# Kernel optimization log

Measured on AMD Instinct MI355X. Metric: run time of the kernel, lower is better.

The kernel has to match this reference:

```python
import jax, jax.numpy as jnp
import numpy as np

# operators = ["min" (T-norm, no_edge offset = 1), "max" (T-conorm, no_edge offset = 0)]
# edge_types = ["identity", "complement", "no_edge"]
NO_EDGE_OFFSET_T_NORM = 1.0
NO_EDGE_OFFSET_T_CONORM = 0.0


def setup_inputs() -> dict:
    key = jax.random.key(0)
    k1, k2, k3 = jax.random.split(key, 3)
    N, IN, OUT, OPS, E = 1024, 512, 256, 2, 3
    eps = 1e-6
    return {
        "x": jax.random.uniform(k1, (N, IN), jnp.float32),
        "edge_logits": jnp.ones((OUT, OPS, IN, E), jnp.float32),
        "op_logits": jnp.ones((OUT, OPS), jnp.float32),
        "u_edge": jax.random.uniform(k2, (OUT, OPS, IN, E), jnp.float32, minval=eps, maxval=1.0 - eps),
        "u_op": jax.random.uniform(k3, (OUT, OPS), jnp.float32, minval=eps, maxval=1.0 - eps),
    }


def _gumbel_softmax_hard(logits, u, axis=-1):
    # Straight-through hard Gumbel-softmax (tau=1), reparameterized with uniform noise u.
    g = -jnp.log(-jnp.log(u))
    y_soft = jax.nn.softmax(logits + g, axis=axis)
    idx = jnp.argmax(y_soft, axis=axis)
    y_hard = jax.nn.one_hot(idx, logits.shape[axis], axis=axis, dtype=y_soft.dtype)
    return y_hard + y_soft - jax.lax.stop_gradient(y_soft)


def reference(x, edge_logits, op_logits, u_edge, u_op):
    # x: [N, I] fuzzy memberships in [0, 1]
    op_edge_sel = _gumbel_softmax_hard(edge_logits, u_edge)  # [O, P, I, E]
    op_sel = _gumbel_softmax_hard(op_logits, u_op)           # [O, P]
    op_idx = jnp.argmax(op_sel, axis=-1)                     # [O], 0 -> min (T-norm), 1 -> max (T-conorm)

    # edge_selection = op_edge_selection[range(O), op_idx]   -> [O, I, E]
    edge_sel = jnp.take_along_axis(op_edge_sel, op_idx[:, None, None, None], axis=1)[:, 0]

    is_tnorm = (op_idx == 0)
    no_edge_off = jnp.where(is_tnorm, NO_EDGE_OFFSET_T_NORM, NO_EDGE_OFFSET_T_CONORM).astype(x.dtype)  # [O]

    # edge type values: identity = x, complement = 1 - x, no_edge = 0 (+ operator offset)
    # edge_values[n, o, i] = max_e edge_sel[o, i, e] * etv[n, o, i, e]
    ev = edge_sel[None, :, :, 0] * x[:, None, :]                          # identity   [N, O, I]
    ev = jnp.maximum(ev, edge_sel[None, :, :, 1] * (1.0 - x)[:, None, :])  # complement
    ev = jnp.maximum(ev, edge_sel[None, :, :, 2] * no_edge_off[None, :, None])  # no_edge

    # operator.value over incoming edges: min for T-norm nodes, max for T-conorm nodes
    mn = jnp.min(ev, axis=-1)  # [N, O]
    mx = jnp.max(ev, axis=-1)  # [N, O]
    return jnp.where(is_tnorm[None, :], mn, mx)
```

## Files before the change

### kernel.cpp

```cpp
#include <hip/hip_runtime.h>
#include <math.h>

#define N_   1024
#define IN_  512
#define OUT_ 256
#define E_   3

__global__ __launch_bounds__(256) void setup_op_kernel(
        const float* __restrict__ op_logits,
        const float* __restrict__ u_op,
        int*   __restrict__ opidx,
        float* __restrict__ signv,
        float* __restrict__ neutral) {
    int o = threadIdx.x;
    float s0 = op_logits[o * 2 + 0] - logf(-logf(u_op[o * 2 + 0]));
    float s1 = op_logits[o * 2 + 1] - logf(-logf(u_op[o * 2 + 1]));
    int p = (s1 > s0) ? 1 : 0;
    opidx[o] = p;
    signv[o] = (p == 0) ? 1.0f : -1.0f;
    neutral[o] = (p == 0) ? 1.0f : 0.0f;
}

__global__ __launch_bounds__(256) void setup_coef_kernel(
        const float* __restrict__ edge_logits,
        const float* __restrict__ u_edge,
        const int*   __restrict__ opidx,
        const float* __restrict__ signv,
        const float* __restrict__ neutral,
        unsigned int* __restrict__ coefT) {
    int o = threadIdx.x;
    int i = blockIdx.x;
    int p = opidx[o];
    long base = (((long)(o * 2 + p)) * IN_ + i) * E_;

    float best = -1e30f;
    int be = 0;
#pragma unroll
    for (int e = 0; e < E_; ++e) {
        float u = u_edge[base + e];
        float sc = edge_logits[base + e] - logf(-logf(u));
        if (sc > best) { best = sc; be = e; }
    }
    float s = signv[o];
    float a, b;
    if (be == 0)      { a = s;    b = 0.0f; }
    else if (be == 1) { a = -s;   b = s;    }
    else              { a = 0.0f; b = s * neutral[o]; }

    unsigned int ua = (__float_as_uint(a) >> 16);
    unsigned int ub = (__float_as_uint(b) & 0xffff0000u);
    coefT[i * OUT_ + o] = ua | ub;
}

template <int NPB, int ISTEPS>
__global__ __launch_bounds__(256) void main_kernel(
        const float* __restrict__ x,
        const unsigned int* __restrict__ coefT,
        const float* __restrict__ signv,
        float* __restrict__ outp,
        int write_final) {
    constexpr int NSPLIT = IN_ / ISTEPS;
    int tid = threadIdx.x;
    int bid = blockIdx.x;
    int ks = bid % NSPLIT;
    int nt = bid / NSPLIT;
    int n0 = nt * NPB;
    int i0 = ks * ISTEPS;

    __shared__ float xT[ISTEPS * NPB];

    for (int k = tid; k < ISTEPS * NPB; k += 256) {
        int r = k / ISTEPS;
        int ii = k % ISTEPS;
        xT[ii * NPB + r] = x[(n0 + r) * IN_ + i0 + ii];
    }
    __syncthreads();

    float acc[NPB];
#pragma unroll
    for (int r = 0; r < NPB; ++r) acc[r] = 2.0f;

    const unsigned int* cp = coefT + (long)i0 * OUT_ + tid;

#pragma unroll 4
    for (int ii = 0; ii < ISTEPS; ++ii) {
        unsigned int c = cp[(long)ii * OUT_];
        float a = __uint_as_float(c << 16);
        float b = __uint_as_float(c & 0xffff0000u);
        const float4* xv = (const float4*)&xT[ii * NPB];
        float4 x0 = xv[0];
        float4 x1 = xv[1];
        acc[0] = fminf(acc[0], fmaf(a, x0.x, b));
        acc[1] = fminf(acc[1], fmaf(a, x0.y, b));
        acc[2] = fminf(acc[2], fmaf(a, x0.z, b));
        acc[3] = fminf(acc[3], fmaf(a, x0.w, b));
        acc[4] = fminf(acc[4], fmaf(a, x1.x, b));
        acc[5] = fminf(acc[5], fmaf(a, x1.y, b));
        acc[6] = fminf(acc[6], fmaf(a, x1.z, b));
        acc[7] = fminf(acc[7], fmaf(a, x1.w, b));
    }

    if (write_final) {
        float s = signv[tid];
#pragma unroll
        for (int r = 0; r < NPB; ++r)
            outp[(n0 + r) * OUT_ + tid] = s * acc[r];
    } else {
#pragma unroll
        for (int r = 0; r < NPB; ++r)
            outp[((long)ks * N_ + (n0 + r)) * OUT_ + tid] = acc[r];
    }
}

__global__ __launch_bounds__(256) void reduce_kernel(
        const float* __restrict__ partial,
        const float* __restrict__ signv,
        float* __restrict__ out,
        int nsplit) {
    int j = blockIdx.x * 256 + threadIdx.x;
    float m = partial[j];
    for (int k = 1; k < nsplit; ++k)
        m = fminf(m, partial[(long)k * (N_ * OUT_) + j]);
    out[j] = signv[j & (OUT_ - 1)] * m;
}

extern "C" void kernel_launch(void* const* d_in, const int* in_sizes, int n_in,
                              void* d_out, int out_size, void* d_ws, size_t ws_size,
                              hipStream_t stream) {
    const float* x           = (const float*)d_in[0];
    const float* edge_logits = (const float*)d_in[1];
    const float* op_logits   = (const float*)d_in[2];
    const float* u_edge      = (const float*)d_in[3];
    const float* u_op        = (const float*)d_in[4];
    float* out = (float*)d_out;

    char* ws = (char*)d_ws;
    int*   opidx   = (int*)(ws);
    float* signv   = (float*)(ws + 1024);
    float* neutral = (float*)(ws + 2048);
    unsigned int* coefT = (unsigned int*)(ws + 4096);
    float* partial = (float*)(ws + 4096 + (size_t)IN_ * OUT_ * 4);

    setup_op_kernel<<<1, 256, 0, stream>>>(op_logits, u_op, opidx, signv, neutral);
    setup_coef_kernel<<<IN_, 256, 0, stream>>>(edge_logits, u_edge, opidx, signv,
                                               neutral, coefT);

    size_t need = 4096 + (size_t)IN_ * OUT_ * 4 + 4ull * N_ * OUT_ * 4;
    if (ws_size >= need) {
        main_kernel<8, 128><<<(N_ / 8) * 4, 256, 0, stream>>>(x, coefT, signv,
                                                              partial, 0);
        reduce_kernel<<<(N_ * OUT_) / 256, 256, 0, stream>>>(partial, signv, out, 4);
    } else {
        main_kernel<8, 512><<<(N_ / 8), 256, 0, stream>>>(x, coefT, signv, out, 1);
    }
}
```

Baseline: 90.89 us.

## Fuse setup kernels and drop split-K partials with reduce pass

Merges the op-selection and coefficient setup kernels into one kernel indexed by output column, so each block recomputes its op choice locally. Replaces the split-K main kernel plus reduce kernel with a single pass of 4 rows per block over the full input dimension, writing the final output directly. This removes two kernel launches and the partial buffer round trip to memory, at the cost of longer per-thread loops and a different grid shape (256 blocks instead of 512). The setup kernel now writes coefT with strided stores across output columns.

```diff
diff --git a/kernel.cpp b/kernel.cpp
--- a/kernel.cpp
+++ b/kernel.cpp
@@ -6,73 +6,63 @@
 #define OUT_ 256
 #define E_   3
 
-__global__ __launch_bounds__(256) void setup_op_kernel(
+__global__ __launch_bounds__(256) void setup_kernel(
+        const float* __restrict__ edge_logits,
         const float* __restrict__ op_logits,
+        const float* __restrict__ u_edge,
         const float* __restrict__ u_op,
-        int*   __restrict__ opidx,
-        float* __restrict__ signv,
-        float* __restrict__ neutral) {
-    int o = threadIdx.x;
+        unsigned int* __restrict__ coefT,
+        float* __restrict__ signv) {
+    int o = blockIdx.x;
+    int t = threadIdx.x;
+
     float s0 = op_logits[o * 2 + 0] - logf(-logf(u_op[o * 2 + 0]));
     float s1 = op_logits[o * 2 + 1] - logf(-logf(u_op[o * 2 + 1]));
     int p = (s1 > s0) ? 1 : 0;
-    opidx[o] = p;
-    signv[o] = (p == 0) ? 1.0f : -1.0f;
-    neutral[o] = (p == 0) ? 1.0f : 0.0f;
+    float s       = (p == 0) ? 1.0f : -1.0f;
+    float neutral = (p == 0) ? 1.0f : 0.0f;
+    if (t == 0) signv[o] = s;
+
+    long rowbase = ((long)(o * 2 + p)) * IN_ * E_;
+
+#pragma unroll
+    for (int rep = 0; rep < IN_ / 256; ++rep) {
+        int i = t + rep * 256;
+        long base = rowbase + (long)i * E_;
+
+        float best = -1e30f;
+        int be = 0;
+#pragma unroll
+        for (int e = 0; e < E_; ++e) {
+            float sc = edge_logits[base + e] - logf(-logf(u_edge[base + e]));
+            if (sc > best) { best = sc; be = e; }
+        }
+        float a, b;
+        if (be == 0)      { a = s;    b = 0.0f;       }
+        else if (be == 1) { a = -s;   b = s;          }
+        else              { a = 0.0f; b = s * neutral; }
+
+        unsigned int ua = (__float_as_uint(a) >> 16);
+        unsigned int ub = (__float_as_uint(b) & 0xffff0000u);
+        coefT[i * OUT_ + o] = ua | ub;
+    }
 }
 
-__global__ __launch_bounds__(256) void setup_coef_kernel(
-        const float* __restrict__ edge_logits,
-        const float* __restrict__ u_edge,
-        const int*   __restrict__ opidx,
-        const float* __restrict__ signv,
-        const float* __restrict__ neutral,
-        unsigned int* __restrict__ coefT) {
-    int o = threadIdx.x;
-    int i = blockIdx.x;
-    int p = opidx[o];
-    long base = (((long)(o * 2 + p)) * IN_ + i) * E_;
-
-    float best = -1e30f;
-    int be = 0;
-#pragma unroll
-    for (int e = 0; e < E_; ++e) {
-        float u = u_edge[base + e];
-        float sc = edge_logits[base + e] - logf(-logf(u));
-        if (sc > best) { best = sc; be = e; }
-    }
-    float s = signv[o];
-    float a, b;
-    if (be == 0)      { a = s;    b = 0.0f; }
-    else if (be == 1) { a = -s;   b = s;    }
-    else              { a = 0.0f; b = s * neutral[o]; }
-
-    unsigned int ua = (__float_as_uint(a) >> 16);
-    unsigned int ub = (__float_as_uint(b) & 0xffff0000u);
-    coefT[i * OUT_ + o] = ua | ub;
-}
-
-template <int NPB, int ISTEPS>
+#define NPB 4
 __global__ __launch_bounds__(256) void main_kernel(
         const float* __restrict__ x,
         const unsigned int* __restrict__ coefT,
         const float* __restrict__ signv,
-        float* __restrict__ outp,
-        int write_final) {
-    constexpr int NSPLIT = IN_ / ISTEPS;
+        float* __restrict__ out) {
     int tid = threadIdx.x;
-    int bid = blockIdx.x;
-    int ks = bid % NSPLIT;
-    int nt = bid / NSPLIT;
-    int n0 = nt * NPB;
-    int i0 = ks * ISTEPS;
+    int n0 = blockIdx.x * NPB;
 
-    __shared__ float xT[ISTEPS * NPB];
+    __shared__ float xT[IN_ * NPB];
 
-    for (int k = tid; k < ISTEPS * NPB; k += 256) {
-        int r = k / ISTEPS;
-        int ii = k % ISTEPS;
-        xT[ii * NPB + r] = x[(n0 + r) * IN_ + i0 + ii];
+    for (int k = tid; k < IN_ * NPB; k += 256) {
+        int r = k >> 9;
+        int ii = k & (IN_ - 1);
+        xT[ii * NPB + r] = x[(n0 + r) * IN_ + ii];
     }
     __syncthreads();
 
@@ -80,48 +70,24 @@
 #pragma unroll
     for (int r = 0; r < NPB; ++r) acc[r] = 2.0f;
 
-    const unsigned int* cp = coefT + (long)i0 * OUT_ + tid;
+    const unsigned int* cp = coefT + tid;
 
-#pragma unroll 4
-    for (int ii = 0; ii < ISTEPS; ++ii) {
-        unsigned int c = cp[(long)ii * OUT_];
+#pragma unroll 8
+    for (int ii = 0; ii < IN_; ++ii) {
+        unsigned int c = cp[ii * OUT_];
         float a = __uint_as_float(c << 16);
         float b = __uint_as_float(c & 0xffff0000u);
-        const float4* xv = (const float4*)&xT[ii * NPB];
-        float4 x0 = xv[0];
-        float4 x1 = xv[1];
-        acc[0] = fminf(acc[0], fmaf(a, x0.x, b));
-        acc[1] = fminf(acc[1], fmaf(a, x0.y, b));
-        acc[2] = fminf(acc[2], fmaf(a, x0.z, b));
-        acc[3] = fminf(acc[3], fmaf(a, x0.w, b));
-        acc[4] = fminf(acc[4], fmaf(a, x1.x, b));
-        acc[5] = fminf(acc[5], fmaf(a, x1.y, b));
-        acc[6] = fminf(acc[6], fmaf(a, x1.z, b));
-        acc[7] = fminf(acc[7], fmaf(a, x1.w, b));
+        float4 xv = *(const float4*)&xT[ii * NPB];
+        acc[0] = fminf(acc[0], fmaf(a, xv.x, b));
+        acc[1] = fminf(acc[1], fmaf(a, xv.y, b));
+        acc[2] = fminf(acc[2], fmaf(a, xv.z, b));
+        acc[3] = fminf(acc[3], fmaf(a, xv.w, b));
     }
 
-    if (write_final) {
-        float s = signv[tid];
+    float s = signv[tid];
 #pragma unroll
-        for (int r = 0; r < NPB; ++r)
-            outp[(n0 + r) * OUT_ + tid] = s * acc[r];
-    } else {
-#pragma unroll
-        for (int r = 0; r < NPB; ++r)
-            outp[((long)ks * N_ + (n0 + r)) * OUT_ + tid] = acc[r];
-    }
-}
-
-__global__ __launch_bounds__(256) void reduce_kernel(
-        const float* __restrict__ partial,
-        const float* __restrict__ signv,
-        float* __restrict__ out,
-        int nsplit) {
-    int j = blockIdx.x * 256 + threadIdx.x;
-    float m = partial[j];
-    for (int k = 1; k < nsplit; ++k)
-        m = fminf(m, partial[(long)k * (N_ * OUT_) + j]);
-    out[j] = signv[j & (OUT_ - 1)] * m;
+    for (int r = 0; r < NPB; ++r)
+        out[(n0 + r) * OUT_ + tid] = s * acc[r];
 }
 
 extern "C" void kernel_launch(void* const* d_in, const int* in_sizes, int n_in,
@@ -135,22 +101,10 @@
     float* out = (float*)d_out;
 
     char* ws = (char*)d_ws;
-    int*   opidx   = (int*)(ws);
-    float* signv   = (float*)(ws + 1024);
-    float* neutral = (float*)(ws + 2048);
-    unsigned int* coefT = (unsigned int*)(ws + 4096);
-    float* partial = (float*)(ws + 4096 + (size_t)IN_ * OUT_ * 4);
+    unsigned int* coefT = (unsigned int*)(ws);
+    float* signv        = (float*)(ws + (size_t)IN_ * OUT_ * 4);
 
-    setup_op_kernel<<<1, 256, 0, stream>>>(op_logits, u_op, opidx, signv, neutral);
-    setup_coef_kernel<<<IN_, 256, 0, stream>>>(edge_logits, u_edge, opidx, signv,
-                                               neutral, coefT);
-
-    size_t need = 4096 + (size_t)IN_ * OUT_ * 4 + 4ull * N_ * OUT_ * 4;
-    if (ws_size >= need) {
-        main_kernel<8, 128><<<(N_ / 8) * 4, 256, 0, stream>>>(x, coefT, signv,
-                                                              partial, 0);
-        reduce_kernel<<<(N_ * OUT_) / 256, 256, 0, stream>>>(partial, signv, out, 4);
-    } else {
-        main_kernel<8, 512><<<(N_ / 8), 256, 0, stream>>>(x, coefT, signv, out, 1);
-    }
+    setup_kernel<<<OUT_, 256, 0, stream>>>(edge_logits, op_logits, u_edge, u_op,
+                                           coefT, signv);
+    main_kernel<<<N_ / NPB, 256, 0, stream>>>(x, coefT, signv, out);
 }
```

Result: slower. 93.62 us (+3.0%).
